# Kernel tuning notes

Measured on AMD Instinct MI355X. Metric: run time of the kernel, lower is better.

The kernel has to match this reference:

```python
import jax, jax.numpy as jnp
import numpy as np

NUM_USERS = 200000
NUM_ITEMS = 100000
EMBED_DIM = 64
N_LAYERS = 3
NNZ = 6000000
BATCH = 16384
N_NODES = NUM_USERS + NUM_ITEMS


def setup_inputs() -> dict:
    key = jax.random.key(0)
    k1, k2, k3, k4, k5, k6, k7 = jax.random.split(key, 7)
    user_emb = 0.01 * jax.random.normal(k1, (NUM_USERS, EMBED_DIM), dtype=jnp.float32)
    item_emb = 0.01 * jax.random.normal(k2, (NUM_ITEMS, EMBED_DIM), dtype=jnp.float32)
    adj_rows = jax.random.randint(k3, (NNZ,), 0, N_NODES, dtype=jnp.int32)
    adj_cols = jax.random.randint(k4, (NNZ,), 0, N_NODES, dtype=jnp.int32)
    # positive normalized-adjacency-like values (roughly 1/deg scale)
    adj_vals = jax.random.uniform(k5, (NNZ,), dtype=jnp.float32) * 0.1
    user_ids = jax.random.randint(k6, (BATCH,), 0, NUM_USERS, dtype=jnp.int32)
    item_ids = jax.random.randint(k7, (BATCH,), 0, NUM_ITEMS, dtype=jnp.int32)
    return {
        "user_emb": user_emb,
        "item_emb": item_emb,
        "adj_rows": adj_rows,
        "adj_cols": adj_cols,
        "adj_vals": adj_vals,
        "user_ids": user_ids,
        "item_ids": item_ids,
    }


def reference(user_emb, item_emb, adj_rows, adj_cols, adj_vals, user_ids, item_ids):
    # propagate: repeated SpMM over adjacency with running accumulation
    all_emb = jnp.concatenate([user_emb, item_emb], axis=0)  # [N, D]
    acc = all_emb  # running sum of layer embeddings (fuses stack+mean)
    x = all_emb
    for _ in range(N_LAYERS):
        # SpMM: x_new[r] = sum_e adj_vals[e] * x[adj_cols[e]] for rows r
        msgs = adj_vals[:, None] * x[adj_cols]  # [nnz, D]
        x = jax.ops.segment_sum(msgs, adj_rows, num_segments=N_NODES)
        acc = acc + x
    mean_emb = acc / jnp.float32(N_LAYERS + 1)  # mean over layer outputs
    user_embs = mean_emb[:NUM_USERS]
    item_embs = mean_emb[NUM_USERS:]
    u = user_embs[user_ids]  # [B, D]
    i = item_embs[item_ids]  # [B, D]
    scores = jnp.sum(u * i, axis=1)  # [B]
    return scores
```

## Files before the change

kernel.cpp:

```cpp
#include <hip/hip_runtime.h>

#define EMBED_DIM 64
#define NBLK_A 256
#define BUCKET_SHIFT 9
#define BUCKET_ROWS 512
#define MAX_NBUCK 640
#define SCAN2_CHUNK 2048
#define COL_BITS 19
#define STAGE_CAP 15360

typedef float fx4 __attribute__((ext_vector_type(4)));
typedef int   ix4 __attribute__((ext_vector_type(4)));
typedef float fv4 __attribute__((ext_vector_type(4)));
typedef _Float16 h8v __attribute__((ext_vector_type(8)));

__global__ void convert_x_kernel(const float* __restrict__ ue, const float* __restrict__ ie,
                                 _Float16* __restrict__ xh, int nu_elems, int total) {
    int i = blockIdx.x * blockDim.x + threadIdx.x;
    int stride = gridDim.x * blockDim.x;
    int n8 = total >> 3;
    int nu8 = nu_elems >> 3;
    for (; i < n8; i += stride) {
        const float4* src = (i < nu8) ? (const float4*)(ue) + 2 * i
                                      : (const float4*)(ie) + 2 * (i - nu8);
        float4 lo = src[0];
        float4 hi = src[1];
        h8v o;
        o[0] = (_Float16)lo.x; o[1] = (_Float16)lo.y;
        o[2] = (_Float16)lo.z; o[3] = (_Float16)lo.w;
        o[4] = (_Float16)hi.x; o[5] = (_Float16)hi.y;
        o[6] = (_Float16)hi.z; o[7] = (_Float16)hi.w;
        reinterpret_cast<h8v*>(xh)[i] = o;
    }
}

__global__ __launch_bounds__(256) void bucket_count_kernel(
    const int* __restrict__ rows, int* __restrict__ blockCounts,
    int nnz, int nbuck, int chunk) {
    __shared__ int hist[MAX_NBUCK];
    int t = threadIdx.x, blk = blockIdx.x;
    for (int i = t; i < nbuck; i += 256) hist[i] = 0;
    __syncthreads();
    int e0 = blk * chunk;
    int e1 = min(e0 + chunk, nnz);
    for (int e = e0 + t * 4; e < e1; e += 1024) {
        ix4 r4 = __builtin_nontemporal_load(reinterpret_cast<const ix4*>(rows + e));
        atomicAdd(&hist[r4.x >> BUCKET_SHIFT], 1);
        atomicAdd(&hist[r4.y >> BUCKET_SHIFT], 1);
        atomicAdd(&hist[r4.z >> BUCKET_SHIFT], 1);
        atomicAdd(&hist[r4.w >> BUCKET_SHIFT], 1);
    }
    __syncthreads();
    for (int u = t; u < nbuck; u += 256)
        blockCounts[u * NBLK_A + blk] = hist[u];
}

__global__ void scan8_phase1(const int* __restrict__ in, int* __restrict__ bsum, int n) {
    __shared__ int wsum[4];
    int t = threadIdx.x, b = blockIdx.x;
    int i0 = b * SCAN2_CHUNK + t * 8;
    int s = 0;
    #pragma unroll
    for (int k = 0; k < 8; ++k) { int i = i0 + k; if (i < n) s += in[i]; }
    #pragma unroll
    for (int off = 1; off < 64; off <<= 1) s += __shfl_xor(s, off);
    if ((t & 63) == 0) wsum[t >> 6] = s;
    __syncthreads();
    if (t == 0) bsum[b] = wsum[0] + wsum[1] + wsum[2] + wsum[3];
}

__global__ void scan_phase2(const int* __restrict__ bsum, int* __restrict__ boff, int nb) {
    __shared__ int lds[512];
    int t = threadIdx.x;
    lds[t] = (t < nb) ? bsum[t] : 0;
    __syncthreads();
    for (int off = 1; off < 512; off <<= 1) {
        int v = (t >= off) ? lds[t - off] : 0;
        __syncthreads();
        lds[t] += v;
        __syncthreads();
    }
    if (t < nb) boff[t] = (t == 0) ? 0 : lds[t - 1];
}

__global__ void scan8_phase3(const int* __restrict__ in, const int* __restrict__ boff,
                             int* __restrict__ out, int n) {
    __shared__ int wexcl[4];
    int t = threadIdx.x, b = blockIdx.x;
    int lane = t & 63, w = t >> 6;
    int i0 = b * SCAN2_CHUNK + t * 8;
    int c[8];
    int s = 0;
    #pragma unroll
    for (int k = 0; k < 8; ++k) { int i = i0 + k; c[k] = (i < n) ? in[i] : 0; s += c[k]; }
    int incl = s;
    #pragma unroll
    for (int off = 1; off < 64; off <<= 1) {
        int u = __shfl_up(incl, off);
        if (lane >= off) incl += u;
    }
    if (lane == 63) wexcl[w] = incl;
    __syncthreads();
    int wbase = 0;
    for (int ww = 0; ww < w; ++ww) wbase += wexcl[ww];
    int run = incl - s + wbase + boff[b];
    #pragma unroll
    for (int k = 0; k < 8; ++k) {
        int i = i0 + k;
        if (i < n) { out[i] = run; run += c[k]; }
    }
}

__global__ __launch_bounds__(256) void bucket_scatter_kernel(
    const int* __restrict__ rows, const int* __restrict__ cols,
    const float* __restrict__ vals, const int* __restrict__ scanOut,
    int2* __restrict__ smeta, int nnz, int nbuck, int chunk) {
    __shared__ int cur[MAX_NBUCK];
    int t = threadIdx.x, blk = blockIdx.x;
    for (int u = t; u < nbuck; u += 256) cur[u] = scanOut[u * NBLK_A + blk];
    __syncthreads();
    int e0 = blk * chunk;
    int e1 = min(e0 + chunk, nnz);
    for (int e = e0 + t * 4; e < e1; e += 1024) {
        ix4 r4 = __builtin_nontemporal_load(reinterpret_cast<const ix4*>(rows + e));
        ix4 c4 = __builtin_nontemporal_load(reinterpret_cast<const ix4*>(cols + e));
        fv4 v4 = __builtin_nontemporal_load(reinterpret_cast<const fv4*>(vals + e));
        int p0 = atomicAdd(&cur[r4.x >> BUCKET_SHIFT], 1);
        smeta[p0] = make_int2(((r4.x & (BUCKET_ROWS - 1)) << COL_BITS) | c4.x, __float_as_int(v4.x));
        int p1 = atomicAdd(&cur[r4.y >> BUCKET_SHIFT], 1);
        smeta[p1] = make_int2(((r4.y & (BUCKET_ROWS - 1)) << COL_BITS) | c4.y, __float_as_int(v4.y));
        int p2 = atomicAdd(&cur[r4.z >> BUCKET_SHIFT], 1);
        smeta[p2] = make_int2(((r4.z & (BUCKET_ROWS - 1)) << COL_BITS) | c4.z, __float_as_int(v4.z));
        int p3 = atomicAdd(&cur[r4.w >> BUCKET_SHIFT], 1);
        smeta[p3] = make_int2(((r4.w & (BUCKET_ROWS - 1)) << COL_BITS) | c4.w, __float_as_int(v4.w));
    }
}

__global__ __launch_bounds__(256) void bucket_build_kernel(
    const int2* __restrict__ smeta, const int* __restrict__ scanOut,
    int2* __restrict__ perm, int* __restrict__ row_ptr,
    int nnz, int n_nodes, int nbuck) {
    __shared__ int hist[BUCKET_ROWS], excl[BUCKET_ROWS], cur[BUCKET_ROWS];
    __shared__ int wex[4];
    __shared__ int2 stage[STAGE_CAP];
    int t = threadIdx.x, b = blockIdx.x;
    int lane = t & 63, w = t >> 6;
    int ebeg = scanOut[b * NBLK_A];
    int eend = (b + 1 < nbuck) ? scanOut[(b + 1) * NBLK_A] : nnz;
    hist[t] = 0; hist[t + 256] = 0;
    __syncthreads();
    for (int e = ebeg + t; e < eend; e += 256)
        atomicAdd(&hist[smeta[e].x >> COL_BITS], 1);
    __syncthreads();
    int a = hist[2 * t], bcnt = hist[2 * t + 1];
    int s = a + bcnt;
    int incl = s;
    #pragma unroll
    for (int off = 1; off < 64; off <<= 1) {
        int u = __shfl_up(incl, off);
        if (lane >= off) incl += u;
    }
    if (lane == 63) wex[w] = incl;
    __syncthreads();
    int wbase = 0;
    for (int ww = 0; ww < w; ++ww) wbase += wex[ww];
    int es = wbase + incl - s;
    excl[2 * t] = es;
    excl[2 * t + 1] = es + a;
    cur[2 * t] = es;
    cur[2 * t + 1] = es + a;
    __syncthreads();
    int base_row = b << BUCKET_SHIFT;
    for (int r = t; r < BUCKET_ROWS; r += 256) {
        int gr = base_row + r;
        if (gr < n_nodes) row_ptr[gr] = ebeg + excl[r];
    }
    if (b == 0 && t == 0) row_ptr[n_nodes] = nnz;
    int nbe = eend - ebeg;
    if (nbe <= STAGE_CAP) {
        for (int e = ebeg + t; e < eend; e += 256) {
            int2 m = smeta[e];
            int l = m.x >> COL_BITS;
            int p = atomicAdd(&cur[l], 1);
            stage[p] = make_int2(m.x & ((1 << COL_BITS) - 1), m.y);
        }
        __syncthreads();
        for (int i = t; i < nbe; i += 256)
            perm[ebeg + i] = stage[i];
    } else {
        for (int e = ebeg + t; e < eend; e += 256) {
            int2 m = smeta[e];
            int l = m.x >> COL_BITS;
            int p = atomicAdd(&cur[l], 1);
            perm[ebeg + p] = make_int2(m.x & ((1 << COL_BITS) - 1), m.y);
        }
    }
}

__global__ void init_bacc_kernel(const float* __restrict__ ue, const float* __restrict__ ie,
                                 const int* __restrict__ uids, const int* __restrict__ iids,
                                 float* __restrict__ uacc, float* __restrict__ iacc, int batch) {
    int t = blockIdx.x * blockDim.x + threadIdx.x;
    if (t >= batch * 16) return;
    int b = t >> 4;
    int q = t & 15;
    const float4* ue4 = (const float4*)ue;
    const float4* ie4 = (const float4*)ie;
    ((float4*)uacc)[t] = ue4[(long)uids[b] * 16 + q];
    ((float4*)iacc)[t] = ie4[(long)iids[b] * 16 + q];
}

__global__ __launch_bounds__(256) void spmm_csr_h_kernel(
    const int* __restrict__ row_ptr, const int2* __restrict__ perm,
    const _Float16* __restrict__ x, _Float16* __restrict__ y, int n_nodes) {
    int lane = threadIdx.x & 63;
    int row = (blockIdx.x * blockDim.x + threadIdx.x) >> 6;
    if (row >= n_nodes) return;
    int start = row_ptr[row];
    int end   = row_ptr[row + 1];
    int sub  = lane >> 3;
    unsigned dimb = ((unsigned)(lane & 7)) << 4;
    const char* xb = reinterpret_cast<const char*>(x);
    float acc0[8], acc1[8];
    #pragma unroll
    for (int k = 0; k < 8; ++k) { acc0[k] = 0.f; acc1[k] = 0.f; }
    for (int base = start; base < end; base += 16) {
        int e0 = base + sub;
        int e1 = e0 + 8;
        int2 p0 = (e0 < end) ? perm[e0] : make_int2(0, 0);
        int2 p1 = (e1 < end) ? perm[e1] : make_int2(0, 0);
        float v0 = __int_as_float(p0.y);
        float v1 = __int_as_float(p1.y);
        h8v xv0 = *reinterpret_cast<const h8v*>(xb + ((((unsigned)p0.x) << 7) | dimb));
        h8v xv1 = *reinterpret_cast<const h8v*>(xb + ((((unsigned)p1.x) << 7) | dimb));
        #pragma unroll
        for (int k = 0; k < 8; ++k) acc0[k] = fmaf(v0, (float)xv0[k], acc0[k]);
        #pragma unroll
        for (int k = 0; k < 8; ++k) acc1[k] = fmaf(v1, (float)xv1[k], acc1[k]);
    }
    float accf[8];
    #pragma unroll
    for (int k = 0; k < 8; ++k) accf[k] = acc0[k] + acc1[k];
    #pragma unroll
    for (int off = 8; off < 64; off <<= 1) {
        #pragma unroll
        for (int k = 0; k < 8; ++k) accf[k] += __shfl_xor(accf[k], off);
    }
    if (sub == 0) {
        h8v o;
        #pragma unroll
        for (int k = 0; k < 8; ++k) o[k] = (_Float16)accf[k];
        *reinterpret_cast<h8v*>(reinterpret_cast<char*>(y) + ((((unsigned)row) << 7) | dimb)) = o;
    }
}

__global__ __launch_bounds__(256) void spmm_batch_h_kernel(
    const int* __restrict__ row_ptr, const int2* __restrict__ perm,
    const _Float16* __restrict__ x,
    const int* __restrict__ uids, const int* __restrict__ iids,
    float* __restrict__ uacc, float* __restrict__ iacc,
    int batch, int num_users) {
    int lane = threadIdx.x & 63;
    int w = (blockIdx.x * blockDim.x + threadIdx.x) >> 6;
    if (w >= 2 * batch) return;
    int row;
    float* target;
    if (w < batch) { row = uids[w];                     target = uacc + (long)w * EMBED_DIM; }
    else           { row = num_users + iids[w - batch]; target = iacc + (long)(w - batch) * EMBED_DIM; }
    int start = row_ptr[row];
    int end   = row_ptr[row + 1];
    int sub  = lane >> 3;
    int dimq = lane & 7;
    unsigned dimb = ((unsigned)dimq) << 4;
    const char* xb = reinterpret_cast<const char*>(x);
    float acc0[8], acc1[8];
    #pragma unroll
    for (int k = 0; k < 8; ++k) { acc0[k] = 0.f; acc1[k] = 0.f; }
    for (int base = start; base < end; base += 16) {
        int e0 = base + sub;
        int e1 = e0 + 8;
        int2 p0 = (e0 < end) ? perm[e0] : make_int2(0, 0);
        int2 p1 = (e1 < end) ? perm[e1] : make_int2(0, 0);
        float v0 = __int_as_float(p0.y);
        float v1 = __int_as_float(p1.y);
        h8v xv0 = *reinterpret_cast<const h8v*>(xb + ((((unsigned)p0.x) << 7) | dimb));
        h8v xv1 = *reinterpret_cast<const h8v*>(xb + ((((unsigned)p1.x) << 7) | dimb));
        #pragma unroll
        for (int k = 0; k < 8; ++k) acc0[k] = fmaf(v0, (float)xv0[k], acc0[k]);
        #pragma unroll
        for (int k = 0; k < 8; ++k) acc1[k] = fmaf(v1, (float)xv1[k], acc1[k]);
    }
    float accf[8];
    #pragma unroll
    for (int k = 0; k < 8; ++k) accf[k] = acc0[k] + acc1[k];
    #pragma unroll
    for (int off = 8; off < 64; off <<= 1) {
        #pragma unroll
        for (int k = 0; k < 8; ++k) accf[k] += __shfl_xor(accf[k], off);
    }
    if (sub == 0) {
        fx4* t4 = reinterpret_cast<fx4*>(target) + dimq * 2;
        fx4 lo = t4[0], hi = t4[1];
        lo.x += accf[0]; lo.y += accf[1]; lo.z += accf[2]; lo.w += accf[3];
        hi.x += accf[4]; hi.y += accf[5]; hi.z += accf[6]; hi.w += accf[7];
        t4[0] = lo; t4[1] = hi;
    }
}

__global__ void bacc_add_h_kernel(const _Float16* __restrict__ y,
                                  const int* __restrict__ uids, const int* __restrict__ iids,
                                  float* __restrict__ uacc, float* __restrict__ iacc,
                                  int batch, int num_users) {
    int t = blockIdx.x * blockDim.x + threadIdx.x;
    if (t >= batch * 8) return;
    int b = t >> 3;
    int q = t & 7;
    const h8v* y8 = (const h8v*)y;
    h8v u = y8[(long)uids[b] * 8 + q];
    h8v v = y8[((long)num_users + iids[b]) * 8 + q];
    float4* ua = (float4*)uacc + (long)b * 16 + q * 2;
    float4* ia = (float4*)iacc + (long)b * 16 + q * 2;
    float4 a0 = ua[0], a1 = ua[1];
    a0.x += (float)u[0]; a0.y += (float)u[1]; a0.z += (float)u[2]; a0.w += (float)u[3];
    a1.x += (float)u[4]; a1.y += (float)u[5]; a1.z += (float)u[6]; a1.w += (float)u[7];
    ua[0] = a0; ua[1] = a1;
    float4 c0 = ia[0], c1 = ia[1];
    c0.x += (float)v[0]; c0.y += (float)v[1]; c0.z += (float)v[2]; c0.w += (float)v[3];
    c1.x += (float)v[4]; c1.y += (float)v[5]; c1.z += (float)v[6]; c1.w += (float)v[7];
    ia[0] = c0; ia[1] = c1;
}

__global__ void score_kernel(const float* __restrict__ uacc, const float* __restrict__ iacc,
                             float* __restrict__ out, int batch) {
    int lane = threadIdx.x & 63;
    int w = (blockIdx.x * blockDim.x + threadIdx.x) >> 6;
    if (w >= batch) return;
    float p = uacc[(long)w * EMBED_DIM + lane] * iacc[(long)w * EMBED_DIM + lane];
    #pragma unroll
    for (int off = 32; off > 0; off >>= 1) p += __shfl_down(p, off);
    if (lane == 0) out[w] = p * (1.0f / 16.0f);
}

extern "C" void kernel_launch(void* const* d_in, const int* in_sizes, int n_in,
                              void* d_out, int out_size, void* d_ws, size_t ws_size,
                              hipStream_t stream) {
    const float* user_emb = (const float*)d_in[0];
    const float* item_emb = (const float*)d_in[1];
    const int*   adj_rows = (const int*)d_in[2];
    const int*   adj_cols = (const int*)d_in[3];
    const float* adj_vals = (const float*)d_in[4];
    const int*   user_ids = (const int*)d_in[5];
    const int*   item_ids = (const int*)d_in[6];
    float* out = (float*)d_out;

    const int num_users = in_sizes[0] / EMBED_DIM;
    const int num_items = in_sizes[1] / EMBED_DIM;
    const int n_nodes   = num_users + num_items;
    const int nnz       = in_sizes[2];
    const int batch     = in_sizes[5];

    const long node_elems = (long)n_nodes * EMBED_DIM;
    const long bacc_elems = (long)batch * EMBED_DIM;

    const int nbuck = (n_nodes + BUCKET_ROWS - 1) >> BUCKET_SHIFT;
    const int nscan = nbuck * NBLK_A;
    const int nscan_blocks = (nscan + SCAN2_CHUNK - 1) / SCAN2_CHUNK;

    char* wp = (char*)d_ws;
    _Float16* xh   = (_Float16*)wp;      wp += node_elems * sizeof(_Float16);
    _Float16* bufA = (_Float16*)wp;      wp += node_elems * sizeof(_Float16);
    _Float16* bufB = (_Float16*)wp;      wp += node_elems * sizeof(_Float16);
    float* uacc = (float*)wp;            wp += bacc_elems * sizeof(float);
    float* iacc = (float*)wp;            wp += bacc_elems * sizeof(float);
    int*   row_ptr = (int*)wp;           wp += (size_t)(n_nodes + 4) * sizeof(int);
    int*   bsum    = (int*)wp;           wp += 512 * sizeof(int);
    int*   boff    = (int*)wp;           wp += 512 * sizeof(int);
    int*   blockCounts = (int*)wp;       wp += (size_t)nscan * sizeof(int);
    int*   scanOut     = (int*)wp;       wp += (size_t)nscan * sizeof(int);
    wp = (char*)(((uintptr_t)wp + 15) & ~(uintptr_t)15);
    int2*  perm    = (int2*)wp;          wp += (size_t)nnz * sizeof(int2);

    int2* smeta = (int2*)bufA;

    const int chunkA = (((nnz + NBLK_A - 1) / NBLK_A) + 1023) & ~1023;

    bucket_count_kernel<<<NBLK_A, 256, 0, stream>>>(adj_rows, blockCounts, nnz, nbuck, chunkA);
    scan8_phase1<<<nscan_blocks, 256, 0, stream>>>(blockCounts, bsum, nscan);
    scan_phase2<<<1, 512, 0, stream>>>(bsum, boff, nscan_blocks);
    scan8_phase3<<<nscan_blocks, 256, 0, stream>>>(blockCounts, boff, scanOut, nscan);
    bucket_scatter_kernel<<<NBLK_A, 256, 0, stream>>>(adj_rows, adj_cols, adj_vals,
                                                      scanOut, smeta, nnz, nbuck, chunkA);
    bucket_build_kernel<<<nbuck, 256, 0, stream>>>(smeta, scanOut, perm,
                                                   row_ptr, nnz, n_nodes, nbuck);

    convert_x_kernel<<<2048, 256, 0, stream>>>(user_emb, item_emb, xh,
                                               num_users * EMBED_DIM, (int)node_elems);

    {
        int blocks = (batch * 16 + 255) / 256;
        init_bacc_kernel<<<blocks, 256, 0, stream>>>(user_emb, item_emb, user_ids, item_ids,
                                                     uacc, iacc, batch);
    }

    const int spmm_blocks = ((n_nodes * 64) + 255) / 256;
    const int bblocks = (batch * 8 + 255) / 256;

    spmm_csr_h_kernel<<<spmm_blocks, 256, 0, stream>>>(row_ptr, perm, xh, bufA, n_nodes);
    bacc_add_h_kernel<<<bblocks, 256, 0, stream>>>(bufA, user_ids, item_ids,
                                                   uacc, iacc, batch, num_users);

    spmm_csr_h_kernel<<<spmm_blocks, 256, 0, stream>>>(row_ptr, perm, bufA, bufB, n_nodes);
    bacc_add_h_kernel<<<bblocks, 256, 0, stream>>>(bufB, user_ids, item_ids,
                                                   uacc, iacc, batch, num_users);

    {
        int waves = 2 * batch;
        int blocks = (waves * 64 + 255) / 256;
        spmm_batch_h_kernel<<<blocks, 256, 0, stream>>>(row_ptr, perm, bufB,
                                                        user_ids, item_ids,
                                                        uacc, iacc, batch, num_users);
    }

    {
        int blocks = (batch * 64 + 255) / 256;
        score_kernel<<<blocks, 256, 0, stream>>>(uacc, iacc, out, batch);
    }
}
```

Before: 497.4 us.

## Prune layer-2 SpMM to batch neighbourhoods and fuse final layer with scoring

A new kernel marks the batch user and item rows plus their direct neighbours in a byte mask. The second full SpMM then skips rows outside that mask, since the third layer only needs those rows. The third-layer batch SpMM is fused with the dot-product scoring, which removes the separate score kernel and the accumulator read-modify-write. The full SpMM loop is also unrolled to three accumulators for more memory-level parallelism. The catch is that with about 20 random neighbours per row the mask likely covers most nodes, while the memset and marking pass add fixed cost.

```diff
diff --git a/kernel.cpp b/kernel.cpp
--- a/kernel.cpp
+++ b/kernel.cpp
@@ -210,37 +210,60 @@
     ((float4*)iacc)[t] = ie4[(long)iids[b] * 16 + q];
 }
 
+__global__ __launch_bounds__(256) void mark_needed_kernel(
+    const int* __restrict__ row_ptr, const int2* __restrict__ perm,
+    const int* __restrict__ uids, const int* __restrict__ iids,
+    char* __restrict__ needed, int batch, int num_users) {
+    int lane = threadIdx.x & 63;
+    int w = (blockIdx.x * blockDim.x + threadIdx.x) >> 6;
+    if (w >= 2 * batch) return;
+    int row = (w < batch) ? uids[w] : num_users + iids[w - batch];
+    if (lane == 0) needed[row] = 1;
+    int start = row_ptr[row];
+    int end   = row_ptr[row + 1];
+    for (int e = start + lane; e < end; e += 64)
+        needed[perm[e].x] = 1;
+}
+
 __global__ __launch_bounds__(256) void spmm_csr_h_kernel(
     const int* __restrict__ row_ptr, const int2* __restrict__ perm,
-    const _Float16* __restrict__ x, _Float16* __restrict__ y, int n_nodes) {
+    const _Float16* __restrict__ x, _Float16* __restrict__ y,
+    const char* __restrict__ needed, int n_nodes) {
     int lane = threadIdx.x & 63;
     int row = (blockIdx.x * blockDim.x + threadIdx.x) >> 6;
     if (row >= n_nodes) return;
+    if (needed && !needed[row]) return;
     int start = row_ptr[row];
     int end   = row_ptr[row + 1];
     int sub  = lane >> 3;
     unsigned dimb = ((unsigned)(lane & 7)) << 4;
     const char* xb = reinterpret_cast<const char*>(x);
-    float acc0[8], acc1[8];
-    #pragma unroll
-    for (int k = 0; k < 8; ++k) { acc0[k] = 0.f; acc1[k] = 0.f; }
-    for (int base = start; base < end; base += 16) {
+    float acc0[8], acc1[8], acc2[8];
+    #pragma unroll
+    for (int k = 0; k < 8; ++k) { acc0[k] = 0.f; acc1[k] = 0.f; acc2[k] = 0.f; }
+    for (int base = start; base < end; base += 24) {
         int e0 = base + sub;
         int e1 = e0 + 8;
+        int e2 = e0 + 16;
         int2 p0 = (e0 < end) ? perm[e0] : make_int2(0, 0);
         int2 p1 = (e1 < end) ? perm[e1] : make_int2(0, 0);
+        int2 p2 = (e2 < end) ? perm[e2] : make_int2(0, 0);
         float v0 = __int_as_float(p0.y);
         float v1 = __int_as_float(p1.y);
+        float v2 = __int_as_float(p2.y);
         h8v xv0 = *reinterpret_cast<const h8v*>(xb + ((((unsigned)p0.x) << 7) | dimb));
         h8v xv1 = *reinterpret_cast<const h8v*>(xb + ((((unsigned)p1.x) << 7) | dimb));
+        h8v xv2 = *reinterpret_cast<const h8v*>(xb + ((((unsigned)p2.x) << 7) | dimb));
         #pragma unroll
         for (int k = 0; k < 8; ++k) acc0[k] = fmaf(v0, (float)xv0[k], acc0[k]);
         #pragma unroll
         for (int k = 0; k < 8; ++k) acc1[k] = fmaf(v1, (float)xv1[k], acc1[k]);
+        #pragma unroll
+        for (int k = 0; k < 8; ++k) acc2[k] = fmaf(v2, (float)xv2[k], acc2[k]);
     }
     float accf[8];
     #pragma unroll
-    for (int k = 0; k < 8; ++k) accf[k] = acc0[k] + acc1[k];
+    for (int k = 0; k < 8; ++k) accf[k] = acc0[k] + acc1[k] + acc2[k];
     #pragma unroll
     for (int off = 8; off < 64; off <<= 1) {
         #pragma unroll
@@ -254,57 +277,84 @@
     }
 }
 
-__global__ __launch_bounds__(256) void spmm_batch_h_kernel(
+__global__ __launch_bounds__(256) void spmm_batch_score_kernel(
     const int* __restrict__ row_ptr, const int2* __restrict__ perm,
     const _Float16* __restrict__ x,
     const int* __restrict__ uids, const int* __restrict__ iids,
-    float* __restrict__ uacc, float* __restrict__ iacc,
-    int batch, int num_users) {
+    const float* __restrict__ uacc, const float* __restrict__ iacc,
+    float* __restrict__ out, int batch, int num_users) {
     int lane = threadIdx.x & 63;
-    int w = (blockIdx.x * blockDim.x + threadIdx.x) >> 6;
-    if (w >= 2 * batch) return;
-    int row;
-    float* target;
-    if (w < batch) { row = uids[w];                     target = uacc + (long)w * EMBED_DIM; }
-    else           { row = num_users + iids[w - batch]; target = iacc + (long)(w - batch) * EMBED_DIM; }
-    int start = row_ptr[row];
-    int end   = row_ptr[row + 1];
+    int b = (blockIdx.x * blockDim.x + threadIdx.x) >> 6;
+    if (b >= batch) return;
     int sub  = lane >> 3;
     int dimq = lane & 7;
     unsigned dimb = ((unsigned)dimq) << 4;
     const char* xb = reinterpret_cast<const char*>(x);
-    float acc0[8], acc1[8];
-    #pragma unroll
-    for (int k = 0; k < 8; ++k) { acc0[k] = 0.f; acc1[k] = 0.f; }
-    for (int base = start; base < end; base += 16) {
-        int e0 = base + sub;
-        int e1 = e0 + 8;
-        int2 p0 = (e0 < end) ? perm[e0] : make_int2(0, 0);
-        int2 p1 = (e1 < end) ? perm[e1] : make_int2(0, 0);
-        float v0 = __int_as_float(p0.y);
-        float v1 = __int_as_float(p1.y);
-        h8v xv0 = *reinterpret_cast<const h8v*>(xb + ((((unsigned)p0.x) << 7) | dimb));
-        h8v xv1 = *reinterpret_cast<const h8v*>(xb + ((((unsigned)p1.x) << 7) | dimb));
-        #pragma unroll
-        for (int k = 0; k < 8; ++k) acc0[k] = fmaf(v0, (float)xv0[k], acc0[k]);
-        #pragma unroll
-        for (int k = 0; k < 8; ++k) acc1[k] = fmaf(v1, (float)xv1[k], acc1[k]);
-    }
-    float accf[8];
-    #pragma unroll
-    for (int k = 0; k < 8; ++k) accf[k] = acc0[k] + acc1[k];
+    float u3[8], i3[8];
+    #pragma unroll
+    for (int k = 0; k < 8; ++k) { u3[k] = 0.f; i3[k] = 0.f; }
+    {
+        int row = uids[b];
+        int start = row_ptr[row];
+        int end   = row_ptr[row + 1];
+        for (int base = start; base < end; base += 16) {
+            int e0 = base + sub;
+            int e1 = e0 + 8;
+            int2 p0 = (e0 < end) ? perm[e0] : make_int2(0, 0);
+            int2 p1 = (e1 < end) ? perm[e1] : make_int2(0, 0);
+            float v0 = __int_as_float(p0.y);
+            float v1 = __int_as_float(p1.y);
+            h8v xv0 = *reinterpret_cast<const h8v*>(xb + ((((unsigned)p0.x) << 7) | dimb));
+            h8v xv1 = *reinterpret_cast<const h8v*>(xb + ((((unsigned)p1.x) << 7) | dimb));
+            #pragma unroll
+            for (int k = 0; k < 8; ++k) u3[k] = fmaf(v0, (float)xv0[k], u3[k]);
+            #pragma unroll
+            for (int k = 0; k < 8; ++k) u3[k] = fmaf(v1, (float)xv1[k], u3[k]);
+        }
+    }
+    {
+        int row = num_users + iids[b];
+        int start = row_ptr[row];
+        int end   = row_ptr[row + 1];
+        for (int base = start; base < end; base += 16) {
+            int e0 = base + sub;
+            int e1 = e0 + 8;
+            int2 p0 = (e0 < end) ? perm[e0] : make_int2(0, 0);
+            int2 p1 = (e1 < end) ? perm[e1] : make_int2(0, 0);
+            float v0 = __int_as_float(p0.y);
+            float v1 = __int_as_float(p1.y);
+            h8v xv0 = *reinterpret_cast<const h8v*>(xb + ((((unsigned)p0.x) << 7) | dimb));
+            h8v xv1 = *reinterpret_cast<const h8v*>(xb + ((((unsigned)p1.x) << 7) | dimb));
+            #pragma unroll
+            for (int k = 0; k < 8; ++k) i3[k] = fmaf(v0, (float)xv0[k], i3[k]);
+            #pragma unroll
+            for (int k = 0; k < 8; ++k) i3[k] = fmaf(v1, (float)xv1[k], i3[k]);
+        }
+    }
     #pragma unroll
     for (int off = 8; off < 64; off <<= 1) {
         #pragma unroll
-        for (int k = 0; k < 8; ++k) accf[k] += __shfl_xor(accf[k], off);
-    }
-    if (sub == 0) {
-        fx4* t4 = reinterpret_cast<fx4*>(target) + dimq * 2;
-        fx4 lo = t4[0], hi = t4[1];
-        lo.x += accf[0]; lo.y += accf[1]; lo.z += accf[2]; lo.w += accf[3];
-        hi.x += accf[4]; hi.y += accf[5]; hi.z += accf[6]; hi.w += accf[7];
-        t4[0] = lo; t4[1] = hi;
-    }
+        for (int k = 0; k < 8; ++k) {
+            u3[k] += __shfl_xor(u3[k], off);
+            i3[k] += __shfl_xor(i3[k], off);
+        }
+    }
+    const fx4* ua = reinterpret_cast<const fx4*>(uacc + (long)b * EMBED_DIM) + dimq * 2;
+    const fx4* ia = reinterpret_cast<const fx4*>(iacc + (long)b * EMBED_DIM) + dimq * 2;
+    fx4 ulo = ua[0], uhi = ua[1];
+    fx4 ilo = ia[0], ihi = ia[1];
+    float s = 0.f;
+    s += (ulo.x + u3[0]) * (ilo.x + i3[0]);
+    s += (ulo.y + u3[1]) * (ilo.y + i3[1]);
+    s += (ulo.z + u3[2]) * (ilo.z + i3[2]);
+    s += (ulo.w + u3[3]) * (ilo.w + i3[3]);
+    s += (uhi.x + u3[4]) * (ihi.x + i3[4]);
+    s += (uhi.y + u3[5]) * (ihi.y + i3[5]);
+    s += (uhi.z + u3[6]) * (ihi.z + i3[6]);
+    s += (uhi.w + u3[7]) * (ihi.w + i3[7]);
+    #pragma unroll
+    for (int off = 1; off < 8; off <<= 1) s += __shfl_xor(s, off);
+    if (lane == 0) out[b] = s * (1.0f / 16.0f);
 }
 
 __global__ void bacc_add_h_kernel(const _Float16* __restrict__ y,
@@ -330,17 +380,6 @@
     ia[0] = c0; ia[1] = c1;
 }
 
-__global__ void score_kernel(const float* __restrict__ uacc, const float* __restrict__ iacc,
-                             float* __restrict__ out, int batch) {
-    int lane = threadIdx.x & 63;
-    int w = (blockIdx.x * blockDim.x + threadIdx.x) >> 6;
-    if (w >= batch) return;
-    float p = uacc[(long)w * EMBED_DIM + lane] * iacc[(long)w * EMBED_DIM + lane];
-    #pragma unroll
-    for (int off = 32; off > 0; off >>= 1) p += __shfl_down(p, off);
-    if (lane == 0) out[w] = p * (1.0f / 16.0f);
-}
-
 extern "C" void kernel_launch(void* const* d_in, const int* in_sizes, int n_in,
                               void* d_out, int out_size, void* d_ws, size_t ws_size,
                               hipStream_t stream) {
@@ -377,6 +416,7 @@
     int*   boff    = (int*)wp;           wp += 512 * sizeof(int);
     int*   blockCounts = (int*)wp;       wp += (size_t)nscan * sizeof(int);
     int*   scanOut     = (int*)wp;       wp += (size_t)nscan * sizeof(int);
+    char*  needed      = wp;             wp += (size_t)n_nodes;
     wp = (char*)(((uintptr_t)wp + 15) & ~(uintptr_t)15);
     int2*  perm    = (int2*)wp;          wp += (size_t)nnz * sizeof(int2);
 
@@ -402,27 +442,32 @@
                                                      uacc, iacc, batch);
     }
 
-    const int spmm_blocks = ((n_nodes * 64) + 255) / 256;
-    const int bblocks = (batch * 8 + 255) / 256;
-
-    spmm_csr_h_kernel<<<spmm_blocks, 256, 0, stream>>>(row_ptr, perm, xh, bufA, n_nodes);
-    bacc_add_h_kernel<<<bblocks, 256, 0, stream>>>(bufA, user_ids, item_ids,
-                                                   uacc, iacc, batch, num_users);
-
-    spmm_csr_h_kernel<<<spmm_blocks, 256, 0, stream>>>(row_ptr, perm, bufA, bufB, n_nodes);
-    bacc_add_h_kernel<<<bblocks, 256, 0, stream>>>(bufB, user_ids, item_ids,
-                                                   uacc, iacc, batch, num_users);
-
+    hipMemsetAsync(needed, 0, (size_t)n_nodes, stream);
     {
         int waves = 2 * batch;
         int blocks = (waves * 64 + 255) / 256;
-        spmm_batch_h_kernel<<<blocks, 256, 0, stream>>>(row_ptr, perm, bufB,
-                                                        user_ids, item_ids,
-                                                        uacc, iacc, batch, num_users);
-    }
+        mark_needed_kernel<<<blocks, 256, 0, stream>>>(row_ptr, perm, user_ids, item_ids,
+                                                       needed, batch, num_users);
+    }
+
+    const int spmm_blocks = ((n_nodes * 64) + 255) / 256;
+    const int bblocks = (batch * 8 + 255) / 256;
+
+    spmm_csr_h_kernel<<<spmm_blocks, 256, 0, stream>>>(row_ptr, perm, xh, bufA,
+                                                       nullptr, n_nodes);
+    bacc_add_h_kernel<<<bblocks, 256, 0, stream>>>(bufA, user_ids, item_ids,
+                                                   uacc, iacc, batch, num_users);
+
+    spmm_csr_h_kernel<<<spmm_blocks, 256, 0, stream>>>(row_ptr, perm, bufA, bufB,
+                                                       needed, n_nodes);
+    bacc_add_h_kernel<<<bblocks, 256, 0, stream>>>(bufB, user_ids, item_ids,
+                                                   uacc, iacc, batch, num_users);
 
     {
         int blocks = (batch * 64 + 255) / 256;
-        score_kernel<<<blocks, 256, 0, stream>>>(uacc, iacc, out, batch);
-    }
-}
+        spmm_batch_score_kernel<<<blocks, 256, 0, stream>>>(row_ptr, perm, bufB,
+                                                            user_ids, item_ids,
+                                                            uacc, iacc, out,
+                                                            batch, num_users);
+    }
+}
```

Result: no change. 495.4 us (-0.4%).
